# Kernel tuning notes

Hardware: AMD Instinct MI355X
Metric: run time of the kernel (lower is better)

Reference implementation:

```python
import jax, jax.numpy as jnp
import numpy as np

D = 768
N_HEADS = 12
D_HEAD = D // N_HEADS


def setup_inputs() -> dict:
    key = jax.random.key(0)
    ks = jax.random.split(key, 7)
    sequences = jax.random.normal(ks[0], (32, 512, D), dtype=jnp.float32)
    s = 1.0 / np.sqrt(D_HEAD)
    Wq = jax.random.uniform(ks[1], (N_HEADS, D_HEAD, D_HEAD), jnp.float32, -s, s)
    Wk = jax.random.uniform(ks[2], (N_HEADS, D_HEAD, D_HEAD), jnp.float32, -s, s)
    Wv = jax.random.uniform(ks[3], (N_HEADS, D_HEAD, D_HEAD), jnp.float32, -s, s)
    bq = jax.random.uniform(ks[4], (N_HEADS, D_HEAD), jnp.float32, -s, s)
    bk = jax.random.uniform(ks[5], (N_HEADS, D_HEAD), jnp.float32, -s, s)
    bv = jax.random.uniform(ks[6], (N_HEADS, D_HEAD), jnp.float32, -s, s)
    return {"sequences": sequences, "Wq": Wq, "Wk": Wk, "Wv": Wv,
            "bq": bq, "bk": bk, "bv": bv}


def reference(sequences, Wq, Wk, Wv, bq, bk, bv):
    b, s, d = sequences.shape
    # split channels into heads: [b, s, h, d_head]
    x = sequences.reshape(b, s, N_HEADS, D_HEAD)
    # per-head linear (block-diagonal QKV); Linear: y = x @ W^T + b
    q = jnp.einsum('bshd,hed->bshe', x, Wq) + bq
    k = jnp.einsum('bshd,hed->bshe', x, Wk) + bk
    v = jnp.einsum('bshd,hed->bshe', x, Wv) + bv
    # NOTE: original module does NOT scale by 1/sqrt(d_head)
    scores = jnp.einsum('bshe,bthe->bhst', q, k)  # [b, h, s, s]
    attn = jax.nn.softmax(scores, axis=-1)
    out = jnp.einsum('bhst,bthe->bshe', attn, v)  # [b, s, h, d_head]
    return out.reshape(b, s, d)
```

## Files before the change

kernel.cpp:

```cpp
#include <hip/hip_runtime.h>
#include <stdint.h>

#define B_ 32
#define S_ 512
#define D_ 768
#define H_ 12
#define DH_ 64

typedef __attribute__((ext_vector_type(8))) short bf16x8;
typedef __attribute__((ext_vector_type(4))) float f32x4;
typedef __attribute__((ext_vector_type(4))) short short4v;

#define WP 72
#define VP 136
#define WS_U 0
#define XS_U 13824
#define KC_U 23040
#define VT_U 32256
#define SMEM_BYTES 81920

__device__ __forceinline__ unsigned short f2bf(float f) {
  uint32_t u = __builtin_bit_cast(uint32_t, f);
  return (unsigned short)((u + 0x7fffu + ((u >> 16) & 1u)) >> 16);
}

__device__ __forceinline__ int sigma(int tile, int r16) {
  return 32 * (tile >> 1) + 8 * (r16 >> 2) + 4 * (tile & 1) + (r16 & 3);
}

__device__ __forceinline__ bf16x8 ldfrag8(const unsigned short* p) {
  return *(const bf16x8*)p;
}

#define MFMA(a, b, c) __builtin_amdgcn_mfma_f32_16x16x32_bf16((a), (b), (c), 0, 0, 0)

extern "C" __global__ void __launch_bounds__(512, 2)
mhsa_mfma(const float* __restrict__ seq, const float* __restrict__ Wq,
          const float* __restrict__ Wk, const float* __restrict__ Wv,
          const float* __restrict__ bq, const float* __restrict__ bk,
          const float* __restrict__ bv, float* __restrict__ out)
{
  extern __shared__ unsigned short lds[];
  unsigned short* Ws = lds + WS_U;
  unsigned short* xs = lds + XS_U;
  unsigned short* Kc = lds + KC_U;
  unsigned short* Vt = lds + VT_U;

  const int tid = threadIdx.x;
  const int lane = tid & 63;
  const int w = tid >> 6;
  const int g = lane >> 4;
  const int r16 = lane & 15;
  const int bh = blockIdx.x;
  const int b = bh / H_;
  const int h = bh - b * H_;
  const int r0 = blockIdx.y * 256;
  const int cb8 = 8 * g;

  const float* seqh = seq + (size_t)b * (S_ * D_) + h * DH_;

  #pragma unroll
  for (int i = 0; i < 24; ++i) {
    int idx = tid + i * 512;
    int row = idx >> 6, col = idx & 63;
    const float* src = (idx < 4096) ? (Wq + h * 4096 + idx)
                     : (idx < 8192) ? (Wk + h * 4096 + (idx - 4096))
                                    : (Wv + h * 4096 + (idx - 8192));
    Ws[row * WP + col] = f2bf(*src);
  }
  __syncthreads();

  bf16x8 wkB[4][2];
  #pragma unroll
  for (int e4 = 0; e4 < 4; ++e4)
    #pragma unroll
    for (int ec = 0; ec < 2; ++ec)
      wkB[e4][ec] = ldfrag8(Ws + (64 + 16 * e4 + r16) * WP + 32 * ec + cb8);
  const int ev = w & 3;
  const int th = w >> 2;
  bf16x8 wvA[2];
  #pragma unroll
  for (int ec = 0; ec < 2; ++ec)
    wvA[ec] = ldfrag8(Ws + (128 + 16 * ev + r16) * WP + 32 * ec + cb8);

  float bk_l[4], bv_l[4];
  #pragma unroll
  for (int e4 = 0; e4 < 4; ++e4) bk_l[e4] = bk[h * 64 + 16 * e4 + r16];
  #pragma unroll
  for (int rr = 0; rr < 4; ++rr) bv_l[rr] = bv[h * 64 + 16 * ev + 4 * g + rr];

  bf16x8 qB[2][2];
  for (int cq = 0; cq < 2; ++cq) {
    __syncthreads();
    #pragma unroll
    for (int i = 0; i < 4; ++i) {
      int idx = tid + i * 512;
      int row = idx >> 4, c4 = (idx & 15) << 2;
      const float4 xv = *(const float4*)(seqh + (size_t)(r0 + cq * 128 + row) * D_ + c4);
      short4v s = {(short)f2bf(xv.x), (short)f2bf(xv.y), (short)f2bf(xv.z), (short)f2bf(xv.w)};
      *(short4v*)(xs + row * WP + c4) = s;
    }
    __syncthreads();
    if (th == cq) {
      const int lr = 32 * ev;
      #pragma unroll
      for (int mt = 0; mt < 2; ++mt) {
        bf16x8 xB[2];
        #pragma unroll
        for (int ec = 0; ec < 2; ++ec)
          xB[ec] = ldfrag8(xs + (lr + 16 * mt + r16) * WP + 32 * ec + cb8);
        f32x4 qt[4];
        #pragma unroll
        for (int e4 = 0; e4 < 4; ++e4) {
          f32x4 acc = {0.f, 0.f, 0.f, 0.f};
          #pragma unroll
          for (int ec = 0; ec < 2; ++ec)
            acc = MFMA(ldfrag8(Ws + (16 * e4 + r16) * WP + 32 * ec + cb8), xB[ec], acc);
          qt[e4] = acc;
        }
        #pragma unroll
        for (int ec2 = 0; ec2 < 2; ++ec2) {
          bf16x8 f;
          #pragma unroll
          for (int j = 0; j < 8; ++j) {
            int e4 = 2 * ec2 + (j >> 2), rr = j & 3;
            f[j] = (short)f2bf(qt[e4][rr] + bq[h * 64 + 16 * e4 + 4 * g + rr]);
          }
          qB[mt][ec2] = f;
        }
      }
    }
  }

  f32x4 O[2][4];
  #pragma unroll
  for (int mt = 0; mt < 2; ++mt)
    #pragma unroll
    for (int e4 = 0; e4 < 4; ++e4) O[mt][e4] = {0.f, 0.f, 0.f, 0.f};
  float m_st[2] = {-1e30f, -1e30f}, l_st[2] = {0.f, 0.f};
  const int m0w = w * 32;

  for (int c = 0; c < 4; ++c) {
    __syncthreads();
    #pragma unroll
    for (int i = 0; i < 4; ++i) {
      int idx = tid + i * 512;
      int row = idx >> 4, c4 = (idx & 15) << 2;
      const float4 xv = *(const float4*)(seqh + (size_t)(c * 128 + row) * D_ + c4);
      short4v s = {(short)f2bf(xv.x), (short)f2bf(xv.y), (short)f2bf(xv.z), (short)f2bf(xv.w)};
      *(short4v*)(xs + row * WP + c4) = s;
    }
    __syncthreads();

    {
      bf16x8 aX[2];
      #pragma unroll
      for (int ec = 0; ec < 2; ++ec)
        aX[ec] = ldfrag8(xs + (w * 16 + r16) * WP + 32 * ec + cb8);
      #pragma unroll
      for (int e4 = 0; e4 < 4; ++e4) {
        f32x4 acc = {0.f, 0.f, 0.f, 0.f};
        #pragma unroll
        for (int ec = 0; ec < 2; ++ec) acc = MFMA(aX[ec], wkB[e4][ec], acc);
        const float bkv = bk_l[e4];
        const int rb = w * 16 + 4 * g;
        const int cs = sigma(e4, r16);
        Kc[(rb + 0) * WP + cs] = f2bf(acc[0] + bkv);
        Kc[(rb + 1) * WP + cs] = f2bf(acc[1] + bkv);
        Kc[(rb + 2) * WP + cs] = f2bf(acc[2] + bkv);
        Kc[(rb + 3) * WP + cs] = f2bf(acc[3] + bkv);
      }
    }
    #pragma unroll
    for (int ttl = 0; ttl < 4; ++ttl) {
      int tt = th * 4 + ttl;
      bf16x8 xB[2];
      #pragma unroll
      for (int ec = 0; ec < 2; ++ec)
        xB[ec] = ldfrag8(xs + (tt * 16 + r16) * WP + 32 * ec + cb8);
      f32x4 acc = {0.f, 0.f, 0.f, 0.f};
      #pragma unroll
      for (int ec = 0; ec < 2; ++ec) acc = MFMA(wvA[ec], xB[ec], acc);
      const int rb = 16 * ev + 4 * g;
      const int cs = sigma(tt, r16);
      Vt[(rb + 0) * VP + cs] = f2bf(acc[0] + bv_l[0]);
      Vt[(rb + 1) * VP + cs] = f2bf(acc[1] + bv_l[1]);
      Vt[(rb + 2) * VP + cs] = f2bf(acc[2] + bv_l[2]);
      Vt[(rb + 3) * VP + cs] = f2bf(acc[3] + bv_l[3]);
    }
    __syncthreads();

    bf16x8 pA[4][2];
    #pragma unroll
    for (int mt = 0; mt < 2; ++mt) {
      f32x4 st[8];
      #pragma unroll
      for (int tt = 0; tt < 8; ++tt) {
        bf16x8 aK[2];
        #pragma unroll
        for (int ec = 0; ec < 2; ++ec)
          aK[ec] = ldfrag8(Kc + (tt * 16 + r16) * WP + 32 * ec + cb8);
        f32x4 acc = {0.f, 0.f, 0.f, 0.f};
        #pragma unroll
        for (int ec = 0; ec < 2; ++ec) acc = MFMA(aK[ec], qB[mt][ec], acc);
        st[tt] = acc;
      }
      float mx = st[0][0];
      #pragma unroll
      for (int tt = 0; tt < 8; ++tt)
        #pragma unroll
        for (int rr = 0; rr < 4; ++rr) mx = fmaxf(mx, st[tt][rr]);
      mx = fmaxf(mx, __shfl_xor(mx, 16, 64));
      mx = fmaxf(mx, __shfl_xor(mx, 32, 64));
      float mn = fmaxf(m_st[mt], mx);
      float al = __expf(m_st[mt] - mn);
      m_st[mt] = mn;
      float sum = 0.f;
      #pragma unroll
      for (int tt = 0; tt < 8; ++tt)
        #pragma unroll
        for (int rr = 0; rr < 4; ++rr) {
          float pv = __expf(st[tt][rr] - mn);
          st[tt][rr] = pv;
          sum += pv;
        }
      sum += __shfl_xor(sum, 16, 64);
      sum += __shfl_xor(sum, 32, 64);
      l_st[mt] = l_st[mt] * al + sum;
      float af[4];
      #pragma unroll
      for (int rr = 0; rr < 4; ++rr) af[rr] = __shfl(al, 4 * g + rr, 64);
      #pragma unroll
      for (int e4 = 0; e4 < 4; ++e4)
        #pragma unroll
        for (int rr = 0; rr < 4; ++rr) O[mt][e4][rr] *= af[rr];
      #pragma unroll
      for (int u = 0; u < 4; ++u) {
        bf16x8 f;
        #pragma unroll
        for (int j = 0; j < 8; ++j) f[j] = (short)f2bf(st[2 * u + (j >> 2)][j & 3]);
        pA[u][mt] = f;
      }
    }
    #pragma unroll
    for (int u = 0; u < 4; ++u) {
      bf16x8 vB[4];
      #pragma unroll
      for (int e4 = 0; e4 < 4; ++e4)
        vB[e4] = ldfrag8(Vt + (16 * e4 + r16) * VP + 32 * u + cb8);
      #pragma unroll
      for (int mt = 0; mt < 2; ++mt)
        #pragma unroll
        for (int e4 = 0; e4 < 4; ++e4)
          O[mt][e4] = MFMA(pA[u][mt], vB[e4], O[mt][e4]);
    }
  }

  #pragma unroll
  for (int mt = 0; mt < 2; ++mt) {
    float inv[4];
    #pragma unroll
    for (int rr = 0; rr < 4; ++rr) inv[rr] = 1.0f / __shfl(l_st[mt], 4 * g + rr, 64);
    #pragma unroll
    for (int e4 = 0; e4 < 4; ++e4)
      #pragma unroll
      for (int rr = 0; rr < 4; ++rr)
        out[(size_t)(b * S_ + r0 + m0w + 16 * mt + 4 * g + rr) * D_ + h * DH_ + 16 * e4 + r16] =
            O[mt][e4][rr] * inv[rr];
  }
}

extern "C" void kernel_launch(void* const* d_in, const int* in_sizes, int n_in,
                              void* d_out, int out_size, void* d_ws, size_t ws_size,
                              hipStream_t stream) {
  const float* seq = (const float*)d_in[0];
  const float* Wq  = (const float*)d_in[1];
  const float* Wk  = (const float*)d_in[2];
  const float* Wv  = (const float*)d_in[3];
  const float* bq  = (const float*)d_in[4];
  const float* bk  = (const float*)d_in[5];
  const float* bv  = (const float*)d_in[6];
  float* outp = (float*)d_out;

  hipFuncSetAttribute((const void*)mhsa_mfma,
                      hipFuncAttributeMaxDynamicSharedMemorySize, SMEM_BYTES);
  dim3 grid(B_ * H_, 2);
  mhsa_mfma<<<grid, 512, SMEM_BYTES, stream>>>(seq, Wq, Wk, Wv, bq, bk, bv, outp);
}
```

Before: 83.08 us.

## Halve block to 4 waves with 64-row KV chunks and smaller LDS footprint

Shrinks the workgroup from 512 to 256 threads, with each wave owning 64 query rows instead of 32, and streams K/V in 64-row chunks over 8 iterations instead of 128-row chunks over 4. LDS drops to about 45KB by reusing the Kc buffer for Wq during Q projection and narrowing the Vt pitch. Wk fragments are now read from LDS inside the loop instead of being held in registers, and PV MFMAs are interleaved into the softmax loop. The aim is higher occupancy (3 blocks per CU) and less register pressure, at the cost of more synchronisation rounds, more K/V projection passes per query and more LDS reads.

```diff
diff --git a/kernel.cpp b/kernel.cpp
--- a/kernel.cpp
+++ b/kernel.cpp
@@ -12,12 +12,12 @@
 typedef __attribute__((ext_vector_type(4))) short short4v;
 
 #define WP 72
-#define VP 136
-#define WS_U 0
-#define XS_U 13824
-#define KC_U 23040
-#define VT_U 32256
-#define SMEM_BYTES 81920
+#define WK_U 0
+#define WV_U 4608
+#define XS_U 9216
+#define KC_U 13824
+#define VT_U 18432
+#define SMEM_BYTES 46080
 
 __device__ __forceinline__ unsigned short f2bf(float f) {
   uint32_t u = __builtin_bit_cast(uint32_t, f);
@@ -34,88 +34,90 @@
 
 #define MFMA(a, b, c) __builtin_amdgcn_mfma_f32_16x16x32_bf16((a), (b), (c), 0, 0, 0)
 
-extern "C" __global__ void __launch_bounds__(512, 2)
+extern "C" __global__ void __launch_bounds__(256, 3)
 mhsa_mfma(const float* __restrict__ seq, const float* __restrict__ Wq,
           const float* __restrict__ Wk, const float* __restrict__ Wv,
           const float* __restrict__ bq, const float* __restrict__ bk,
           const float* __restrict__ bv, float* __restrict__ out)
 {
   extern __shared__ unsigned short lds[];
-  unsigned short* Ws = lds + WS_U;
-  unsigned short* xs = lds + XS_U;
-  unsigned short* Kc = lds + KC_U;
-  unsigned short* Vt = lds + VT_U;
+  unsigned short* Wkl = lds + WK_U;
+  unsigned short* Wvl = lds + WV_U;
+  unsigned short* xs  = lds + XS_U;
+  unsigned short* Kc  = lds + KC_U;
+  unsigned short* Vt  = lds + VT_U;
 
   const int tid = threadIdx.x;
   const int lane = tid & 63;
   const int w = tid >> 6;
   const int g = lane >> 4;
   const int r16 = lane & 15;
+  const int cb8 = 8 * g;
   const int bh = blockIdx.x;
   const int b = bh / H_;
   const int h = bh - b * H_;
   const int r0 = blockIdx.y * 256;
-  const int cb8 = 8 * g;
 
   const float* seqh = seq + (size_t)b * (S_ * D_) + h * DH_;
 
   #pragma unroll
-  for (int i = 0; i < 24; ++i) {
-    int idx = tid + i * 512;
-    int row = idx >> 6, col = idx & 63;
-    const float* src = (idx < 4096) ? (Wq + h * 4096 + idx)
-                     : (idx < 8192) ? (Wk + h * 4096 + (idx - 4096))
-                                    : (Wv + h * 4096 + (idx - 8192));
-    Ws[row * WP + col] = f2bf(*src);
-  }
+  for (int i = 0; i < 4; ++i) {
+    int fidx = tid + i * 256;
+    int row = fidx >> 4, c4 = (fidx & 15) << 2;
+    {
+      const float4 v = *(const float4*)(Wk + h * 4096 + row * 64 + c4);
+      short4v s = {(short)f2bf(v.x), (short)f2bf(v.y), (short)f2bf(v.z), (short)f2bf(v.w)};
+      *(short4v*)(Wkl + row * WP + c4) = s;
+    }
+    {
+      const float4 v = *(const float4*)(Wv + h * 4096 + row * 64 + c4);
+      short4v s = {(short)f2bf(v.x), (short)f2bf(v.y), (short)f2bf(v.z), (short)f2bf(v.w)};
+      *(short4v*)(Wvl + row * WP + c4) = s;
+    }
+    {
+      const float4 v = *(const float4*)(Wq + h * 4096 + row * 64 + c4);
+      short4v s = {(short)f2bf(v.x), (short)f2bf(v.y), (short)f2bf(v.z), (short)f2bf(v.w)};
+      *(short4v*)(Kc + row * WP + c4) = s;
+    }
+  }
+
+  float bk_l[4], bv_l[4];
+  #pragma unroll
+  for (int e4 = 0; e4 < 4; ++e4) bk_l[e4] = bk[h * 64 + 16 * e4 + r16];
+  #pragma unroll
+  for (int rr = 0; rr < 4; ++rr) bv_l[rr] = bv[h * 64 + 16 * w + 4 * g + rr];
   __syncthreads();
 
-  bf16x8 wkB[4][2];
-  #pragma unroll
-  for (int e4 = 0; e4 < 4; ++e4)
-    #pragma unroll
-    for (int ec = 0; ec < 2; ++ec)
-      wkB[e4][ec] = ldfrag8(Ws + (64 + 16 * e4 + r16) * WP + 32 * ec + cb8);
-  const int ev = w & 3;
-  const int th = w >> 2;
   bf16x8 wvA[2];
   #pragma unroll
   for (int ec = 0; ec < 2; ++ec)
-    wvA[ec] = ldfrag8(Ws + (128 + 16 * ev + r16) * WP + 32 * ec + cb8);
-
-  float bk_l[4], bv_l[4];
-  #pragma unroll
-  for (int e4 = 0; e4 < 4; ++e4) bk_l[e4] = bk[h * 64 + 16 * e4 + r16];
-  #pragma unroll
-  for (int rr = 0; rr < 4; ++rr) bv_l[rr] = bv[h * 64 + 16 * ev + 4 * g + rr];
-
-  bf16x8 qB[2][2];
-  for (int cq = 0; cq < 2; ++cq) {
-    __syncthreads();
+    wvA[ec] = ldfrag8(Wvl + (16 * w + r16) * WP + 32 * ec + cb8);
+
+  bf16x8 qB[4][2];
+  for (int cq = 0; cq < 4; ++cq) {
     #pragma unroll
     for (int i = 0; i < 4; ++i) {
-      int idx = tid + i * 512;
-      int row = idx >> 4, c4 = (idx & 15) << 2;
-      const float4 xv = *(const float4*)(seqh + (size_t)(r0 + cq * 128 + row) * D_ + c4);
+      int fidx = tid + i * 256;
+      int row = fidx >> 4, c4 = (fidx & 15) << 2;
+      const float4 xv = *(const float4*)(seqh + (size_t)(r0 + cq * 64 + row) * D_ + c4);
       short4v s = {(short)f2bf(xv.x), (short)f2bf(xv.y), (short)f2bf(xv.z), (short)f2bf(xv.w)};
       *(short4v*)(xs + row * WP + c4) = s;
     }
     __syncthreads();
-    if (th == cq) {
-      const int lr = 32 * ev;
-      #pragma unroll
-      for (int mt = 0; mt < 2; ++mt) {
+    if (w == cq) {
+      #pragma unroll
+      for (int mt = 0; mt < 4; ++mt) {
         bf16x8 xB[2];
         #pragma unroll
         for (int ec = 0; ec < 2; ++ec)
-          xB[ec] = ldfrag8(xs + (lr + 16 * mt + r16) * WP + 32 * ec + cb8);
+          xB[ec] = ldfrag8(xs + (16 * mt + r16) * WP + 32 * ec + cb8);
         f32x4 qt[4];
         #pragma unroll
         for (int e4 = 0; e4 < 4; ++e4) {
           f32x4 acc = {0.f, 0.f, 0.f, 0.f};
           #pragma unroll
           for (int ec = 0; ec < 2; ++ec)
-            acc = MFMA(ldfrag8(Ws + (16 * e4 + r16) * WP + 32 * ec + cb8), xB[ec], acc);
+            acc = MFMA(ldfrag8(Kc + (16 * e4 + r16) * WP + 32 * ec + cb8), xB[ec], acc);
           qt[e4] = acc;
         }
         #pragma unroll
@@ -130,23 +132,23 @@
         }
       }
     }
-  }
-
-  f32x4 O[2][4];
-  #pragma unroll
-  for (int mt = 0; mt < 2; ++mt)
+    __syncthreads();
+  }
+
+  f32x4 O[4][4];
+  #pragma unroll
+  for (int mt = 0; mt < 4; ++mt)
     #pragma unroll
     for (int e4 = 0; e4 < 4; ++e4) O[mt][e4] = {0.f, 0.f, 0.f, 0.f};
-  float m_st[2] = {-1e30f, -1e30f}, l_st[2] = {0.f, 0.f};
-  const int m0w = w * 32;
-
-  for (int c = 0; c < 4; ++c) {
-    __syncthreads();
+  float m_st[4] = {-1e30f, -1e30f, -1e30f, -1e30f};
+  float l_st[4] = {0.f, 0.f, 0.f, 0.f};
+
+  for (int c = 0; c < 8; ++c) {
     #pragma unroll
     for (int i = 0; i < 4; ++i) {
-      int idx = tid + i * 512;
-      int row = idx >> 4, c4 = (idx & 15) << 2;
-      const float4 xv = *(const float4*)(seqh + (size_t)(c * 128 + row) * D_ + c4);
+      int fidx = tid + i * 256;
+      int row = fidx >> 4, c4 = (fidx & 15) << 2;
+      const float4 xv = *(const float4*)(seqh + (size_t)(c * 64 + row) * D_ + c4);
       short4v s = {(short)f2bf(xv.x), (short)f2bf(xv.y), (short)f2bf(xv.z), (short)f2bf(xv.w)};
       *(short4v*)(xs + row * WP + c4) = s;
     }
@@ -161,7 +163,8 @@
       for (int e4 = 0; e4 < 4; ++e4) {
         f32x4 acc = {0.f, 0.f, 0.f, 0.f};
         #pragma unroll
-        for (int ec = 0; ec < 2; ++ec) acc = MFMA(aX[ec], wkB[e4][ec], acc);
+        for (int ec = 0; ec < 2; ++ec)
+          acc = MFMA(aX[ec], ldfrag8(Wkl + (16 * e4 + r16) * WP + 32 * ec + cb8), acc);
         const float bkv = bk_l[e4];
         const int rb = w * 16 + 4 * g;
         const int cs = sigma(e4, r16);
@@ -172,8 +175,7 @@
       }
     }
     #pragma unroll
-    for (int ttl = 0; ttl < 4; ++ttl) {
-      int tt = th * 4 + ttl;
+    for (int tt = 0; tt < 4; ++tt) {
       bf16x8 xB[2];
       #pragma unroll
       for (int ec = 0; ec < 2; ++ec)
@@ -181,21 +183,20 @@
       f32x4 acc = {0.f, 0.f, 0.f, 0.f};
       #pragma unroll
       for (int ec = 0; ec < 2; ++ec) acc = MFMA(wvA[ec], xB[ec], acc);
-      const int rb = 16 * ev + 4 * g;
+      const int rb = 16 * w + 4 * g;
       const int cs = sigma(tt, r16);
-      Vt[(rb + 0) * VP + cs] = f2bf(acc[0] + bv_l[0]);
-      Vt[(rb + 1) * VP + cs] = f2bf(acc[1] + bv_l[1]);
-      Vt[(rb + 2) * VP + cs] = f2bf(acc[2] + bv_l[2]);
-      Vt[(rb + 3) * VP + cs] = f2bf(acc[3] + bv_l[3]);
-    }
-    __syncthreads();
-
-    bf16x8 pA[4][2];
-    #pragma unroll
-    for (int mt = 0; mt < 2; ++mt) {
-      f32x4 st[8];
-      #pragma unroll
-      for (int tt = 0; tt < 8; ++tt) {
+      Vt[(rb + 0) * WP + cs] = f2bf(acc[0] + bv_l[0]);
+      Vt[(rb + 1) * WP + cs] = f2bf(acc[1] + bv_l[1]);
+      Vt[(rb + 2) * WP + cs] = f2bf(acc[2] + bv_l[2]);
+      Vt[(rb + 3) * WP + cs] = f2bf(acc[3] + bv_l[3]);
+    }
+    __syncthreads();
+
+    #pragma unroll
+    for (int mt = 0; mt < 4; ++mt) {
+      f32x4 st[4];
+      #pragma unroll
+      for (int tt = 0; tt < 4; ++tt) {
         bf16x8 aK[2];
         #pragma unroll
         for (int ec = 0; ec < 2; ++ec)
@@ -207,7 +208,7 @@
       }
       float mx = st[0][0];
       #pragma unroll
-      for (int tt = 0; tt < 8; ++tt)
+      for (int tt = 0; tt < 4; ++tt)
         #pragma unroll
         for (int rr = 0; rr < 4; ++rr) mx = fmaxf(mx, st[tt][rr]);
       mx = fmaxf(mx, __shfl_xor(mx, 16, 64));
@@ -217,7 +218,7 @@
       m_st[mt] = mn;
       float sum = 0.f;
       #pragma unroll
-      for (int tt = 0; tt < 8; ++tt)
+      for (int tt = 0; tt < 4; ++tt)
         #pragma unroll
         for (int rr = 0; rr < 4; ++rr) {
           float pv = __expf(st[tt][rr] - mn);
@@ -235,29 +236,21 @@
         #pragma unroll
         for (int rr = 0; rr < 4; ++rr) O[mt][e4][rr] *= af[rr];
       #pragma unroll
-      for (int u = 0; u < 4; ++u) {
+      for (int u = 0; u < 2; ++u) {
         bf16x8 f;
         #pragma unroll
         for (int j = 0; j < 8; ++j) f[j] = (short)f2bf(st[2 * u + (j >> 2)][j & 3]);
-        pA[u][mt] = f;
-      }
-    }
-    #pragma unroll
-    for (int u = 0; u < 4; ++u) {
-      bf16x8 vB[4];
-      #pragma unroll
-      for (int e4 = 0; e4 < 4; ++e4)
-        vB[e4] = ldfrag8(Vt + (16 * e4 + r16) * VP + 32 * u + cb8);
-      #pragma unroll
-      for (int mt = 0; mt < 2; ++mt)
-        #pragma unroll
-        for (int e4 = 0; e4 < 4; ++e4)
-          O[mt][e4] = MFMA(pA[u][mt], vB[e4], O[mt][e4]);
-    }
-  }
-
-  #pragma unroll
-  for (int mt = 0; mt < 2; ++mt) {
+        #pragma unroll
+        for (int e4 = 0; e4 < 4; ++e4) {
+          bf16x8 vB = ldfrag8(Vt + (16 * e4 + r16) * WP + 32 * u + cb8);
+          O[mt][e4] = MFMA(f, vB, O[mt][e4]);
+        }
+      }
+    }
+  }
+
+  #pragma unroll
+  for (int mt = 0; mt < 4; ++mt) {
     float inv[4];
     #pragma unroll
     for (int rr = 0; rr < 4; ++rr) inv[rr] = 1.0f / __shfl(l_st[mt], 4 * g + rr, 64);
@@ -265,7 +258,7 @@
     for (int e4 = 0; e4 < 4; ++e4)
       #pragma unroll
       for (int rr = 0; rr < 4; ++rr)
-        out[(size_t)(b * S_ + r0 + m0w + 16 * mt + 4 * g + rr) * D_ + h * DH_ + 16 * e4 + r16] =
+        out[(size_t)(b * S_ + r0 + w * 64 + 16 * mt + 4 * g + rr) * D_ + h * DH_ + 16 * e4 + r16] =
             O[mt][e4][rr] * inv[rr];
   }
 }
@@ -285,5 +278,5 @@
   hipFuncSetAttribute((const void*)mhsa_mfma,
                       hipFuncAttributeMaxDynamicSharedMemorySize, SMEM_BYTES);
   dim3 grid(B_ * H_, 2);
-  mhsa_mfma<<<grid, 512, SMEM_BYTES, stream>>>(seq, Wq, Wk, Wv, bq, bk, bv, outp);
-}
+  mhsa_mfma<<<grid, 256, SMEM_BYTES, stream>>>(seq, Wq, Wk, Wv, bq, bk, bv, outp);
+}
```

Result: slower. 204.2 us (+145.8%).
